# Kernel optimization log

Measured on AMD Instinct MI355X. Metric: run time of the kernel, lower is better.

Reference implementation:

```python
import jax, jax.numpy as jnp
import numpy as np

B, N, EMBED, CHEB_K, INP, HID = 32, 8192, 16, 2, 2, 64


def setup_inputs() -> dict:
    key = jax.random.key(0)
    k1, k2, k3, k4 = jax.random.split(key, 4)
    return {
        "x": jax.random.normal(k1, (B, N, INP), dtype=jnp.float32),
        "adj": jax.random.normal(k2, (N, EMBED), dtype=jnp.float32),
        "weights_pool": jax.random.normal(k3, (EMBED, CHEB_K, INP, HID), dtype=jnp.float32) * 0.1,
        "bias_pool": jax.random.normal(k4, (EMBED, HID), dtype=jnp.float32) * 0.1,
    }


def reference(x, adj, weights_pool, bias_pool):
    n = adj.shape[0]
    cheb_k = weights_pool.shape[1]
    # adaptive adjacency: row-softmax of relu(E E^T)
    ADJ = jax.nn.softmax(jax.nn.relu(adj @ adj.T), axis=1)  # [n, n]
    support_set = [jnp.eye(n, dtype=x.dtype), ADJ]
    for k in range(2, cheb_k):  # Chebyshev recursion (fixed small k)
        support_set.append(2.0 * ADJ @ support_set[-1] - support_set[-2])
    supports = jnp.stack(support_set, axis=0)  # [k, n, n]
    # node-adaptive weights / bias
    weights = jnp.einsum("nd,dkio->nkio", adj, weights_pool)  # [n,k,inp,hid]
    bias = adj @ bias_pool  # [n, hid]
    # graph propagation, directly in bnkc layout (fuses the permute)
    x_g = jnp.einsum("knm,bmc->bnkc", supports, x)  # [b,n,k,inp]
    out = jnp.einsum("bnki,nkio->bno", x_g, weights) + bias  # [b,n,hid]
    return out
```

## Files before the change

kernel.cpp:

```cpp
#include <hip/hip_runtime.h>

#define NN 8192
#define BB 32
#define EMB 16
#define HID 64

typedef __attribute__((ext_vector_type(8))) short bf16x8;
typedef __attribute__((ext_vector_type(4))) float f32x4;

static __device__ inline unsigned short f2b(float f) {
    union { float f; unsigned u; } v; v.f = f;
    return (unsigned short)((v.u + 0x7fffu + ((v.u >> 16) & 1u)) >> 16);
}

static __device__ inline unsigned packbf(unsigned e_even, unsigned e_odd) {
#if __has_builtin(__builtin_amdgcn_perm)
    return __builtin_amdgcn_perm(e_odd, e_even, 0x07060302u);
#else
    return (e_odd & 0xFFFF0000u) | (e_even >> 16);
#endif
}

__global__ void k_build(const float* __restrict__ x, const float* __restrict__ adj,
                        short* __restrict__ VTf, short* __restrict__ Afrag,
                        short* __restrict__ adjS) {
    const int t = threadIdx.x;
    const int bx = blockIdx.x;
    if (bx < 256) {
        const int c = bx;
        const int u = t >> 6, lane = t & 63, l = lane & 15, q = lane >> 4;
        const int j = 16 * u + l, b = j >> 1, ch = j & 1;
        const int m0 = 32 * c + 8 * q;
        const float* xp = x + (size_t)b * (NN * 2) + m0 * 2;
        uint4 d;
        unsigned dd[4];
#pragma unroll
        for (int i = 0; i < 4; ++i) {
            float4 xx = *(const float4*)(xp + 4 * i);
            float v0 = ch ? xx.y : xx.x;
            float v1 = ch ? xx.w : xx.z;
            dd[i] = (unsigned)f2b(v0) | ((unsigned)f2b(v1) << 16);
        }
        d.x = dd[0]; d.y = dd[1]; d.z = dd[2]; d.w = dd[3];
        *(uint4*)(VTf + ((size_t)(c * 4 + u) * 64 + lane) * 8) = d;
    } else if (bx < 384) {
        const int cc = t >> 7, tt = t & 127;
        const int c = (bx - 256) * 2 + cc;
        const int h = tt >> 6, lane = tt & 63, l = lane & 15, q = lane >> 4;
        const int row = 32 * c + 8 * (l >> 2) + (l & 3) + 4 * h;
        const float* ap = adj + (size_t)row * EMB + (q & 1) * 8;
        float4 a0 = *(const float4*)(ap);
        float4 a1 = *(const float4*)(ap + 4);
        uint4 d;
        d.x = (unsigned)f2b(a0.x) | ((unsigned)f2b(a0.y) << 16);
        d.y = (unsigned)f2b(a0.z) | ((unsigned)f2b(a0.w) << 16);
        d.z = (unsigned)f2b(a1.x) | ((unsigned)f2b(a1.y) << 16);
        d.w = (unsigned)f2b(a1.z) | ((unsigned)f2b(a1.w) << 16);
        *(uint4*)(Afrag + ((size_t)(c * 2 + h) * 64 + lane) * 8) = d;
    } else {
        const float L2E = 1.4426950408889634f;
        int idx = (bx - 384) * 256 + t;
        float4 aa = *(const float4*)(adj + (size_t)idx * 4);
        uint2 us;
        us.x = (unsigned)f2b(aa.x * L2E) | ((unsigned)f2b(aa.y * L2E) << 16);
        us.y = (unsigned)f2b(aa.z * L2E) | ((unsigned)f2b(aa.w * L2E) << 16);
        *(uint2*)(adjS + (size_t)idx * 4) = us;
    }
}

__launch_bounds__(512, 1)
__global__ void k_main(const short* __restrict__ Afrag, const short* __restrict__ adjS,
                       const short* __restrict__ VTf,
                       float* __restrict__ gnum, float* __restrict__ gden) {
    const int t = threadIdx.x;
    const int wv = t >> 6;
    const int lane = t & 63;
    const int l = lane & 15;
    const int q = lane >> 4;
    const int tile = blockIdx.x & 127;
    const int mh = blockIdx.x >> 7;
    const int n0 = tile * 64;
    const int cbeg = mh * 128 + wv * 16;
    const int cend = cbeg + 16;

    __shared__ __align__(16) unsigned short ysl[8][64][68];
    __shared__ float dsl[8][64];

    bf16x8 Bn[4];
    bf16x8 zv = {0, 0, 0, 0, 0, 0, 0, 0};
#pragma unroll
    for (int s = 0; s < 4; ++s) {
        const short* src = adjS + (size_t)(n0 + 16 * s + l) * EMB + (q & 1) * 8;
        bf16x8 v = *(const bf16x8*)src;
        Bn[s] = (q < 2) ? v : zv;
    }
    const short one = (short)0x3F80;
    bf16x8 ones = {one, one, one, one, one, one, one, one};

    f32x4 acc[4][4];
    f32x4 dacc[4];
#pragma unroll
    for (int u = 0; u < 4; ++u)
#pragma unroll
        for (int s = 0; s < 4; ++s) { acc[u][s][0] = acc[u][s][1] = acc[u][s][2] = acc[u][s][3] = 0.f; }
#pragma unroll
    for (int s = 0; s < 4; ++s) { dacc[s][0] = dacc[s][1] = dacc[s][2] = dacc[s][3] = 0.f; }

    const short* Ap = Afrag + (size_t)lane * 8;
    const short* Vp = VTf + (size_t)lane * 8;

    bf16x8 aCur0 = *(const bf16x8*)(Ap + (size_t)cbeg * 1024);
    bf16x8 aCur1 = *(const bf16x8*)(Ap + (size_t)cbeg * 1024 + 512);

    for (int cg = cbeg; cg < cend; ++cg) {
        bf16x8 v0 = *(const bf16x8*)(Vp + (size_t)cg * 2048);
        bf16x8 v1 = *(const bf16x8*)(Vp + (size_t)cg * 2048 + 512);
        bf16x8 v2 = *(const bf16x8*)(Vp + (size_t)cg * 2048 + 1024);
        bf16x8 v3 = *(const bf16x8*)(Vp + (size_t)cg * 2048 + 1536);
        const int cgn = (cg + 1 < cend) ? cg + 1 : cbeg;
        bf16x8 aN0 = *(const bf16x8*)(Ap + (size_t)cgn * 1024);
        bf16x8 aN1 = *(const bf16x8*)(Ap + (size_t)cgn * 1024 + 512);

        f32x4 z = {0.f, 0.f, 0.f, 0.f};
        f32x4 S0[4], S1[4];
#pragma unroll
        for (int s = 0; s < 4; ++s) {
            S0[s] = __builtin_amdgcn_mfma_f32_16x16x32_bf16(aCur0, Bn[s], z, 0, 0, 0);
            S1[s] = __builtin_amdgcn_mfma_f32_16x16x32_bf16(aCur1, Bn[s], z, 0, 0, 0);
        }
#pragma unroll
        for (int s = 0; s < 4; ++s) {
            unsigned w0[4], w1[4];
#pragma unroll
            for (int r = 0; r < 4; ++r) {
                union { float f; unsigned u; } p0, p1;
                p0.f = __builtin_amdgcn_exp2f(fmaxf(S0[s][r], 0.f));
                p1.f = __builtin_amdgcn_exp2f(fmaxf(S1[s][r], 0.f));
                w0[r] = p0.u;
                w1[r] = p1.u;
            }
            union { bf16x8 v; unsigned d[4]; } pf;
            pf.d[0] = packbf(w0[0], w0[1]);
            pf.d[1] = packbf(w0[2], w0[3]);
            pf.d[2] = packbf(w1[0], w1[1]);
            pf.d[3] = packbf(w1[2], w1[3]);
            acc[0][s] = __builtin_amdgcn_mfma_f32_16x16x32_bf16(v0, pf.v, acc[0][s], 0, 0, 0);
            acc[1][s] = __builtin_amdgcn_mfma_f32_16x16x32_bf16(v1, pf.v, acc[1][s], 0, 0, 0);
            acc[2][s] = __builtin_amdgcn_mfma_f32_16x16x32_bf16(v2, pf.v, acc[2][s], 0, 0, 0);
            acc[3][s] = __builtin_amdgcn_mfma_f32_16x16x32_bf16(v3, pf.v, acc[3][s], 0, 0, 0);
            dacc[s] = __builtin_amdgcn_mfma_f32_16x16x32_bf16(ones, pf.v, dacc[s], 0, 0, 0);
        }
        aCur0 = aN0;
        aCur1 = aN1;
    }

#pragma unroll
    for (int s = 0; s < 4; ++s) {
        const int nl_w = 16 * s + l;
#pragma unroll
        for (int u = 0; u < 4; ++u) {
            union { float f; unsigned u; } a0, a1, a2, a3;
            a0.f = acc[u][s][0]; a1.f = acc[u][s][1]; a2.f = acc[u][s][2]; a3.f = acc[u][s][3];
            uint2 pk;
            pk.x = packbf(a0.u, a1.u);
            pk.y = packbf(a2.u, a3.u);
            *(uint2*)&ysl[wv][nl_w][16 * u + 4 * q] = pk;
        }
        if (q == 0) dsl[wv][nl_w] = dacc[s][0];
    }
    __syncthreads();

    float* gn = gnum + (size_t)(mh * 128 + tile) * 64 * 64;
    float* gd = gden + (size_t)(mh * 128 + tile) * 64;
    const int nl = t >> 4, og = t & 15;
#pragma unroll
    for (int h = 0; h < 2; ++h) {
        const int nr = nl + 32 * h;
        f32x4 ysum = {0.f, 0.f, 0.f, 0.f};
        float dsum = 0.f;
#pragma unroll
        for (int s = 0; s < 8; ++s) {
            ushort4 p = *(const ushort4*)&ysl[s][nr][og * 4];
            union { unsigned u; float f; } c0, c1, c2, c3;
            c0.u = (unsigned)p.x << 16; c1.u = (unsigned)p.y << 16;
            c2.u = (unsigned)p.z << 16; c3.u = (unsigned)p.w << 16;
            ysum[0] += c0.f; ysum[1] += c1.f; ysum[2] += c2.f; ysum[3] += c3.f;
            dsum += dsl[s][nr];
        }
        *(f32x4*)(gn + (size_t)nr * 64 + og * 4) = ysum;
        if (og == 0) gd[nr] = dsum;
    }
}

__global__ void k_epi2(const float* __restrict__ adj, const float* __restrict__ wp,
                       const float* __restrict__ bp, const float* __restrict__ x,
                       const float* __restrict__ gnum, const float* __restrict__ gden,
                       float* __restrict__ out) {
    const int t = threadIdx.x;
    const int nl = t >> 4, og = t & 15;
    const int tile = blockIdx.x >> 1;
    const int half = blockIdx.x & 1;
    const int n0 = blockIdx.x * 32;
    const int nloc = half * 32 + nl;
    const int n = n0 + nl;

    __shared__ float wpl[EMB][5][64];
    __shared__ float adjl[32][EMB];
    __shared__ float xl[32][68];
    __shared__ float ylf[32][68];

    for (int i = t; i < EMB * 5 * 64; i += 512) {
        const int d = i / 320, r = i % 320, c = r >> 6, j = r & 63;
        wpl[d][c][j] = (c < 4) ? wp[(size_t)(d * 4 + c) * 64 + j] : bp[(size_t)d * 64 + j];
    }
    adjl[nl][og] = adj[(size_t)(n0 + nl) * EMB + og];

    const float* gn0 = gnum + (size_t)tile * 64 * 64;
    const float* gn1 = gnum + (size_t)(128 + tile) * 64 * 64;
    f32x4 y0 = *(const f32x4*)(gn0 + (size_t)nloc * 64 + og * 4);
    f32x4 y1 = *(const f32x4*)(gn1 + (size_t)nloc * 64 + og * 4);
    float dsum = gden[(size_t)tile * 64 + nloc] + gden[(size_t)(128 + tile) * 64 + nloc];
    float rden = 1.f / dsum;
    ylf[nl][og * 4 + 0] = (y0[0] + y1[0]) * rden;
    ylf[nl][og * 4 + 1] = (y0[1] + y1[1]) * rden;
    ylf[nl][og * 4 + 2] = (y0[2] + y1[2]) * rden;
    ylf[nl][og * 4 + 3] = (y0[3] + y1[3]) * rden;

    float2 x0 = *(const float2*)(x + ((size_t)(og * 2) * NN + n) * 2);
    float2 x1v = *(const float2*)(x + ((size_t)(og * 2 + 1) * NN + n) * 2);
    xl[nl][og * 4 + 0] = x0.x; xl[nl][og * 4 + 1] = x0.y;
    xl[nl][og * 4 + 2] = x1v.x; xl[nl][og * 4 + 3] = x1v.y;
    __syncthreads();

    float4 W[5];
#pragma unroll
    for (int c = 0; c < 5; ++c) { W[c].x = W[c].y = W[c].z = W[c].w = 0.f; }
#pragma unroll
    for (int d = 0; d < EMB; ++d) {
        const float a = adjl[nl][d];
#pragma unroll
        for (int c = 0; c < 5; ++c) {
            const float4 p = *(const float4*)&wpl[d][c][og * 4];
            W[c].x += a * p.x; W[c].y += a * p.y; W[c].z += a * p.z; W[c].w += a * p.w;
        }
    }

#pragma unroll 4
    for (int b = 0; b < BB; ++b) {
        float xb0 = xl[nl][2 * b], xb1 = xl[nl][2 * b + 1];
        float yb0 = ylf[nl][2 * b], yb1 = ylf[nl][2 * b + 1];
        f32x4 o4;
        o4[0] = xb0 * W[0].x + xb1 * W[1].x + yb0 * W[2].x + yb1 * W[3].x + W[4].x;
        o4[1] = xb0 * W[0].y + xb1 * W[1].y + yb0 * W[2].y + yb1 * W[3].y + W[4].y;
        o4[2] = xb0 * W[0].z + xb1 * W[1].z + yb0 * W[2].z + yb1 * W[3].z + W[4].z;
        o4[3] = xb0 * W[0].w + xb1 * W[1].w + yb0 * W[2].w + yb1 * W[3].w + W[4].w;
        __builtin_nontemporal_store(o4, (f32x4*)(out + ((size_t)b * NN + n) * HID + og * 4));
    }
}

extern "C" void kernel_launch(void* const* d_in, const int* in_sizes, int n_in,
                              void* d_out, int out_size, void* d_ws, size_t ws_size,
                              hipStream_t stream) {
    const float* x   = (const float*)d_in[0];
    const float* adj = (const float*)d_in[1];
    const float* wp  = (const float*)d_in[2];
    const float* bp  = (const float*)d_in[3];
    float* out = (float*)d_out;

    char* w = (char*)d_ws;
    short* VTf   = (short*)w;
    short* Afrag = VTf + (size_t)256 * 4 * 64 * 8;
    short* adjS  = Afrag + (size_t)256 * 2 * 64 * 8;
    float* gnum  = (float*)(adjS + (size_t)NN * EMB);
    float* gden  = gnum + (size_t)256 * 64 * 64;

    k_build<<<512, 256, 0, stream>>>(x, adj, VTf, Afrag, adjS);
    k_main<<<256, 512, 0, stream>>>(Afrag, adjS, VTf, gnum, gden);
    k_epi2<<<256, 512, 0, stream>>>(adj, wp, bp, x, gnum, gden, out);
}
```

Measured before the change: 111.4 us.

## Widen node tile to 128 and compute softmax denominator with VALU sums

The main kernel now covers 128 nodes per block and splits the key dimension into four quarters instead of two, so each wave handles 8 key chunks over 8 node sub-tiles. This reuses each loaded A/V fragment across twice as many nodes, cutting global fragment traffic per unit of work. The denominator MFMA against a ones vector is replaced by per-lane float sums of the exponentials, reduced with cross-lane shuffles, which frees matrix-core issue slots. In exchange, register pressure roughly doubles (32 accumulators), the partial-sum buffer grows, and the epilogue must sum four partials instead of two.

```diff
diff --git a/kernel.cpp b/kernel.cpp
--- a/kernel.cpp
+++ b/kernel.cpp
@@ -77,34 +77,32 @@
     const int lane = t & 63;
     const int l = lane & 15;
     const int q = lane >> 4;
-    const int tile = blockIdx.x & 127;
-    const int mh = blockIdx.x >> 7;
-    const int n0 = tile * 64;
-    const int cbeg = mh * 128 + wv * 16;
-    const int cend = cbeg + 16;
-
-    __shared__ __align__(16) unsigned short ysl[8][64][68];
-    __shared__ float dsl[8][64];
-
-    bf16x8 Bn[4];
+    const int tile = blockIdx.x & 63;
+    const int mq = blockIdx.x >> 6;
+    const int n0 = tile * 128;
+    const int cbeg = mq * 64 + wv * 8;
+    const int cend = cbeg + 8;
+
+    __shared__ __align__(16) unsigned short ysl[8][128][68];
+    __shared__ float dsl[8][128];
+
+    bf16x8 Bn[8];
     bf16x8 zv = {0, 0, 0, 0, 0, 0, 0, 0};
 #pragma unroll
-    for (int s = 0; s < 4; ++s) {
+    for (int s = 0; s < 8; ++s) {
         const short* src = adjS + (size_t)(n0 + 16 * s + l) * EMB + (q & 1) * 8;
         bf16x8 v = *(const bf16x8*)src;
         Bn[s] = (q < 2) ? v : zv;
     }
-    const short one = (short)0x3F80;
-    bf16x8 ones = {one, one, one, one, one, one, one, one};
-
-    f32x4 acc[4][4];
-    f32x4 dacc[4];
+
+    f32x4 acc[4][8];
+    float pden[8];
 #pragma unroll
     for (int u = 0; u < 4; ++u)
 #pragma unroll
-        for (int s = 0; s < 4; ++s) { acc[u][s][0] = acc[u][s][1] = acc[u][s][2] = acc[u][s][3] = 0.f; }
-#pragma unroll
-    for (int s = 0; s < 4; ++s) { dacc[s][0] = dacc[s][1] = dacc[s][2] = dacc[s][3] = 0.f; }
+        for (int s = 0; s < 8; ++s) { acc[u][s][0] = acc[u][s][1] = acc[u][s][2] = acc[u][s][3] = 0.f; }
+#pragma unroll
+    for (int s = 0; s < 8; ++s) pden[s] = 0.f;
 
     const short* Ap = Afrag + (size_t)lane * 8;
     const short* Vp = VTf + (size_t)lane * 8;
@@ -121,24 +119,23 @@
         bf16x8 aN0 = *(const bf16x8*)(Ap + (size_t)cgn * 1024);
         bf16x8 aN1 = *(const bf16x8*)(Ap + (size_t)cgn * 1024 + 512);
 
-        f32x4 z = {0.f, 0.f, 0.f, 0.f};
-        f32x4 S0[4], S1[4];
-#pragma unroll
-        for (int s = 0; s < 4; ++s) {
-            S0[s] = __builtin_amdgcn_mfma_f32_16x16x32_bf16(aCur0, Bn[s], z, 0, 0, 0);
-            S1[s] = __builtin_amdgcn_mfma_f32_16x16x32_bf16(aCur1, Bn[s], z, 0, 0, 0);
-        }
-#pragma unroll
-        for (int s = 0; s < 4; ++s) {
+        const f32x4 z = {0.f, 0.f, 0.f, 0.f};
+#pragma unroll
+        for (int s = 0; s < 8; ++s) {
+            f32x4 S0 = __builtin_amdgcn_mfma_f32_16x16x32_bf16(aCur0, Bn[s], z, 0, 0, 0);
+            f32x4 S1 = __builtin_amdgcn_mfma_f32_16x16x32_bf16(aCur1, Bn[s], z, 0, 0, 0);
             unsigned w0[4], w1[4];
+            float psum = 0.f;
 #pragma unroll
             for (int r = 0; r < 4; ++r) {
                 union { float f; unsigned u; } p0, p1;
-                p0.f = __builtin_amdgcn_exp2f(fmaxf(S0[s][r], 0.f));
-                p1.f = __builtin_amdgcn_exp2f(fmaxf(S1[s][r], 0.f));
+                p0.f = __builtin_amdgcn_exp2f(fmaxf(S0[r], 0.f));
+                p1.f = __builtin_amdgcn_exp2f(fmaxf(S1[r], 0.f));
+                psum += p0.f + p1.f;
                 w0[r] = p0.u;
                 w1[r] = p1.u;
             }
+            pden[s] += psum;
             union { bf16x8 v; unsigned d[4]; } pf;
             pf.d[0] = packbf(w0[0], w0[1]);
             pf.d[1] = packbf(w0[2], w0[3]);
@@ -148,14 +145,21 @@
             acc[1][s] = __builtin_amdgcn_mfma_f32_16x16x32_bf16(v1, pf.v, acc[1][s], 0, 0, 0);
             acc[2][s] = __builtin_amdgcn_mfma_f32_16x16x32_bf16(v2, pf.v, acc[2][s], 0, 0, 0);
             acc[3][s] = __builtin_amdgcn_mfma_f32_16x16x32_bf16(v3, pf.v, acc[3][s], 0, 0, 0);
-            dacc[s] = __builtin_amdgcn_mfma_f32_16x16x32_bf16(ones, pf.v, dacc[s], 0, 0, 0);
         }
         aCur0 = aN0;
         aCur1 = aN1;
     }
 
 #pragma unroll
-    for (int s = 0; s < 4; ++s) {
+    for (int s = 0; s < 8; ++s) {
+        float d = pden[s];
+        d += __shfl_xor(d, 16, 64);
+        d += __shfl_xor(d, 32, 64);
+        pden[s] = d;
+    }
+
+#pragma unroll
+    for (int s = 0; s < 8; ++s) {
         const int nl_w = 16 * s + l;
 #pragma unroll
         for (int u = 0; u < 4; ++u) {
@@ -166,15 +170,15 @@
             pk.y = packbf(a2.u, a3.u);
             *(uint2*)&ysl[wv][nl_w][16 * u + 4 * q] = pk;
         }
-        if (q == 0) dsl[wv][nl_w] = dacc[s][0];
+        if (q == 0) dsl[wv][nl_w] = pden[s];
     }
     __syncthreads();
 
-    float* gn = gnum + (size_t)(mh * 128 + tile) * 64 * 64;
-    float* gd = gden + (size_t)(mh * 128 + tile) * 64;
+    float* gn = gnum + (size_t)(mq * 64 + tile) * 128 * 64;
+    float* gd = gden + (size_t)(mq * 64 + tile) * 128;
     const int nl = t >> 4, og = t & 15;
 #pragma unroll
-    for (int h = 0; h < 2; ++h) {
+    for (int h = 0; h < 4; ++h) {
         const int nr = nl + 32 * h;
         f32x4 ysum = {0.f, 0.f, 0.f, 0.f};
         float dsum = 0.f;
@@ -192,16 +196,15 @@
     }
 }
 
-__global__ void k_epi2(const float* __restrict__ adj, const float* __restrict__ wp,
+__global__ void k_epi3(const float* __restrict__ adj, const float* __restrict__ wp,
                        const float* __restrict__ bp, const float* __restrict__ x,
                        const float* __restrict__ gnum, const float* __restrict__ gden,
                        float* __restrict__ out) {
     const int t = threadIdx.x;
     const int nl = t >> 4, og = t & 15;
-    const int tile = blockIdx.x >> 1;
-    const int half = blockIdx.x & 1;
+    const int tile = blockIdx.x >> 2;
     const int n0 = blockIdx.x * 32;
-    const int nloc = half * 32 + nl;
+    const int nloc = (blockIdx.x & 3) * 32 + nl;
     const int n = n0 + nl;
 
     __shared__ float wpl[EMB][5][64];
@@ -215,16 +218,20 @@
     }
     adjl[nl][og] = adj[(size_t)(n0 + nl) * EMB + og];
 
-    const float* gn0 = gnum + (size_t)tile * 64 * 64;
-    const float* gn1 = gnum + (size_t)(128 + tile) * 64 * 64;
-    f32x4 y0 = *(const f32x4*)(gn0 + (size_t)nloc * 64 + og * 4);
-    f32x4 y1 = *(const f32x4*)(gn1 + (size_t)nloc * 64 + og * 4);
-    float dsum = gden[(size_t)tile * 64 + nloc] + gden[(size_t)(128 + tile) * 64 + nloc];
+    f32x4 ysum = {0.f, 0.f, 0.f, 0.f};
+    float dsum = 0.f;
+#pragma unroll
+    for (int mqi = 0; mqi < 4; ++mqi) {
+        const float* gn = gnum + (size_t)(mqi * 64 + tile) * 128 * 64;
+        f32x4 y = *(const f32x4*)(gn + (size_t)nloc * 64 + og * 4);
+        ysum[0] += y[0]; ysum[1] += y[1]; ysum[2] += y[2]; ysum[3] += y[3];
+        dsum += gden[(size_t)(mqi * 64 + tile) * 128 + nloc];
+    }
     float rden = 1.f / dsum;
-    ylf[nl][og * 4 + 0] = (y0[0] + y1[0]) * rden;
-    ylf[nl][og * 4 + 1] = (y0[1] + y1[1]) * rden;
-    ylf[nl][og * 4 + 2] = (y0[2] + y1[2]) * rden;
-    ylf[nl][og * 4 + 3] = (y0[3] + y1[3]) * rden;
+    ylf[nl][og * 4 + 0] = ysum[0] * rden;
+    ylf[nl][og * 4 + 1] = ysum[1] * rden;
+    ylf[nl][og * 4 + 2] = ysum[2] * rden;
+    ylf[nl][og * 4 + 3] = ysum[3] * rden;
 
     float2 x0 = *(const float2*)(x + ((size_t)(og * 2) * NN + n) * 2);
     float2 x1v = *(const float2*)(x + ((size_t)(og * 2 + 1) * NN + n) * 2);
@@ -272,9 +279,9 @@
     short* Afrag = VTf + (size_t)256 * 4 * 64 * 8;
     short* adjS  = Afrag + (size_t)256 * 2 * 64 * 8;
     float* gnum  = (float*)(adjS + (size_t)NN * EMB);
-    float* gden  = gnum + (size_t)256 * 64 * 64;
+    float* gden  = gnum + (size_t)256 * 128 * 64;
 
     k_build<<<512, 256, 0, stream>>>(x, adj, VTf, Afrag, adjS);
     k_main<<<256, 512, 0, stream>>>(Afrag, adjS, VTf, gnum, gden);
-    k_epi2<<<256, 512, 0, stream>>>(adj, wp, bp, x, gnum, gden, out);
-}
+    k_epi3<<<256, 512, 0, stream>>>(adj, wp, bp, x, gnum, gden, out);
+}
```

Measured after the change: 113.4 us. No clear change (+1.7%).
